# Kernel optimization log

Hardware: AMD Instinct MI355X
Metric: run time of the kernel (lower is better)

## Reference

```python
import jax, jax.numpy as jnp
import numpy as np

B, S, D = 4, 2048, 1024
E, K, H = 8, 2, 2048  # experts, top_k, swiglu hidden (ff_multiplier=2.0)
EPS = 1e-8
RMS_EPS = 1e-6
ROPE_BASE = 10000.0


def setup_inputs() -> dict:
    key = jax.random.key(0)
    ks = jax.random.split(key, 6)
    scale_in = 1.0 / np.sqrt(D)
    scale_h = 1.0 / np.sqrt(H)
    return {
        "x": jax.random.normal(ks[0], (B, S, D), jnp.float32),
        "norm_w": jnp.ones((D,), jnp.float32),
        "router_W": jax.random.normal(ks[1], (E, D), jnp.float32) * scale_in,  # nn.Linear weight [E,D]
        "w1": jax.random.normal(ks[2], (E, H, D), jnp.float32) * scale_in,  # gate proj per expert
        "w3": jax.random.normal(ks[3], (E, H, D), jnp.float32) * scale_in,  # up proj per expert
        "w2": jax.random.normal(ks[4], (E, D, H), jnp.float32) * scale_h,   # down proj per expert
    }


def _rmsnorm(x, w):
    var = jnp.mean(jnp.square(x), axis=-1, keepdims=True)
    return x * jax.lax.rsqrt(var + RMS_EPS) * w


def _rope(x):
    # half-split rotary embedding over full embed dim; x: [B,S,D]
    d2 = D // 2
    inv_freq = 1.0 / (ROPE_BASE ** (jnp.arange(0, d2, dtype=jnp.float32) / d2))
    ang = jnp.arange(S, dtype=jnp.float32)[:, None] * inv_freq[None, :]  # [S,D/2]
    cos, sin = jnp.cos(ang), jnp.sin(ang)
    x1, x2 = x[..., :d2], x[..., d2:]
    return jnp.concatenate([x1 * cos - x2 * sin, x1 * sin + x2 * cos], axis=-1)


def reference(x, norm_w, router_W, w1, w3, w2):
    hidden = _rope(_rmsnorm(x, norm_w))  # [B,S,D]
    logits = jnp.einsum("bsd,ed->bse", hidden, router_W)
    probs = jax.nn.softmax(logits, axis=-1)
    # sparse top-k renormalized gates
    top_v, top_i = jax.lax.top_k(probs, K)  # [B,S,K]
    sparse = jnp.sum(jax.nn.one_hot(top_i, E, dtype=probs.dtype) * top_v[..., None], axis=-2)  # [B,S,E]
    gates = sparse / jnp.clip(jnp.sum(sparse, axis=-1, keepdims=True), EPS)
    # dense all-expert SwiGLU
    g = jnp.einsum("bsd,ehd->bseh", hidden, w1)
    u = jnp.einsum("bsd,ehd->bseh", hidden, w3)
    act = jax.nn.silu(g) * u
    expert_out = jnp.einsum("bseh,edh->bsed", act, w2)  # [B,S,E,D]
    mixed = jnp.sum(gates[..., None] * expert_out, axis=-2)
    return mixed + x
```

## Files before the change

### kernel.cpp

```cpp
#include <hip/hip_runtime.h>

#define TOKENS 8192
#define Dm 1024
#define Hm 2048
#define Sm 2048
#define D2 512
#define SLOTS 16384
#define PADU 128
#define SLOTPAD (SLOTS + 8*PADU)
#define NWE 16777216

#define OF_TAB 0ull
#define OF_HID (OF_TAB + (size_t)Sm*D2*8)
#define OF_ACT (OF_HID + (size_t)TOKENS*Dm*2)
#define OF_W1B (OF_ACT + (size_t)SLOTPAD*Hm*2)
#define OF_W3B (OF_W1B + (size_t)NWE*2)
#define OF_W2B (OF_W3B + (size_t)NWE*2)
#define OF_T2I (OF_W2B + (size_t)NWE*2)
#define OF_T2G (OF_T2I + (size_t)TOKENS*2*4)
#define OF_T2S (OF_T2G + (size_t)TOKENS*2*4)
#define OF_ST  (OF_T2S + (size_t)TOKENS*2*4)
#define OF_SG  (OF_ST + (size_t)SLOTPAD*4)
#define OF_MT  (OF_SG + (size_t)SLOTPAD*4)
#define OF_SO  (OF_MT + 1024)

typedef __bf16 bf16x8 __attribute__((ext_vector_type(8)));
typedef short  s16x8  __attribute__((ext_vector_type(8)));
typedef float  f32x4  __attribute__((ext_vector_type(4)));

__device__ __forceinline__ unsigned short f2bf(float f) {
    union { float f; unsigned u; } v; v.f = f;
    unsigned r = v.u + 0x7fffu + ((v.u >> 16) & 1u);
    return (unsigned short)(r >> 16);
}

__device__ __forceinline__ float bf2f(unsigned short u) {
    union { unsigned u; float f; } v; v.u = ((unsigned)u) << 16;
    return v.f;
}

__device__ __forceinline__ f32x4 mfma16(s16x8 a, s16x8 b, f32x4 c) {
    return __builtin_amdgcn_mfma_f32_16x16x32_bf16(
        __builtin_bit_cast(bf16x8, a), __builtin_bit_cast(bf16x8, b), c, 0, 0, 0);
}

__device__ __forceinline__ void gld16(const void* g, void* l) {
    __builtin_amdgcn_global_load_lds(
        (const __attribute__((address_space(1))) void*)g,
        (__attribute__((address_space(3))) void*)l, 16, 0, 0);
}

__device__ __forceinline__ int xcd_swz(int bid, int nwg) {
    int cpx = nwg >> 3;
    return (bid & 7) * cpx + (bid >> 3);
}

__global__ void k_init(int* slot_token, int* meta) {
    int i = blockIdx.x * 256 + threadIdx.x;
    if (i < SLOTPAD) slot_token[i] = -1;
    if (i < 8) meta[i] = 0;
}

__global__ __launch_bounds__(256) void k_convert3(
    const float* __restrict__ w1, const float* __restrict__ w3,
    const float* __restrict__ w2, unsigned short* __restrict__ d1,
    unsigned short* __restrict__ d3, unsigned short* __restrict__ d2)
{
    size_t i = ((size_t)blockIdx.x * 256 + threadIdx.x) * 8;
    const float* s; unsigned short* d;
    if (i < (size_t)NWE)            { s = w1; d = d1; }
    else if (i < 2ull * NWE)        { s = w3; d = d3; i -= (size_t)NWE; }
    else                            { s = w2; d = d2; i -= 2ull * NWE; }
    float4 a = *(const float4*)(s + i);
    float4 b = *(const float4*)(s + i + 4);
    s16x8 v;
    v[0]=(short)f2bf(a.x); v[1]=(short)f2bf(a.y); v[2]=(short)f2bf(a.z); v[3]=(short)f2bf(a.w);
    v[4]=(short)f2bf(b.x); v[5]=(short)f2bf(b.y); v[6]=(short)f2bf(b.z); v[7]=(short)f2bf(b.w);
    *(s16x8*)(d + i) = v;
}

__global__ void k_table(float2* tab) {
    int i = blockIdx.x * 256 + threadIdx.x;
    int s = i >> 9, j = i & 511;
    float inv = expf(-(float)j * (9.210340371976184f / 512.0f));
    float ang = (float)s * inv;
    tab[i] = make_float2(cosf(ang), sinf(ang));
}

__global__ __launch_bounds__(256) void k_token(
    const float* __restrict__ x, const float* __restrict__ nw,
    const float* __restrict__ rW, const float2* __restrict__ tab,
    unsigned short* __restrict__ hid,
    int* __restrict__ t2i, float* __restrict__ t2g)
{
    int t = blockIdx.x;
    int tid = threadIdx.x;
    int lane = tid & 63, wid = tid >> 6;
    int s = t & (Sm - 1);
    const float* xr = x + (size_t)t * Dm;

    float v0 = xr[tid], v1 = xr[tid + 256], v2 = xr[tid + 512], v3 = xr[tid + 768];
    float ss = v0*v0 + v1*v1 + v2*v2 + v3*v3;
    #pragma unroll
    for (int o = 32; o; o >>= 1) ss += __shfl_down(ss, o);
    __shared__ float red[4];
    if (lane == 0) red[wid] = ss;
    __syncthreads();
    float tot = red[0] + red[1] + red[2] + red[3];
    float rms = rsqrtf(tot * (1.0f / Dm) + 1e-6f);

    float n0 = v0 * rms * nw[tid];
    float n1 = v1 * rms * nw[tid + 256];
    float n2 = v2 * rms * nw[tid + 512];
    float n3 = v3 * rms * nw[tid + 768];

    float2 c0 = tab[s * D2 + tid];
    float2 c1 = tab[s * D2 + tid + 256];
    float h0 = n0 * c0.x - n2 * c0.y;
    float h2 = n0 * c0.y + n2 * c0.x;
    float h1 = n1 * c1.x - n3 * c1.y;
    float h3 = n1 * c1.y + n3 * c1.x;

    size_t base = (size_t)t * Dm;
    hid[base + tid]       = f2bf(h0);
    hid[base + tid + 256] = f2bf(h1);
    hid[base + tid + 512] = f2bf(h2);
    hid[base + tid + 768] = f2bf(h3);

    float p[8];
    #pragma unroll
    for (int e = 0; e < 8; e++) {
        const float* r = rW + (size_t)e * Dm;
        p[e] = h0 * r[tid] + h1 * r[tid + 256] + h2 * r[tid + 512] + h3 * r[tid + 768];
    }
    #pragma unroll
    for (int e = 0; e < 8; e++)
        #pragma unroll
        for (int o = 32; o; o >>= 1) p[e] += __shfl_down(p[e], o);
    __shared__ float rl[4][8];
    if (lane == 0) {
        #pragma unroll
        for (int e = 0; e < 8; e++) rl[wid][e] = p[e];
    }
    __syncthreads();
    if (tid == 0) {
        float lg[8];
        #pragma unroll
        for (int e = 0; e < 8; e++) lg[e] = rl[0][e] + rl[1][e] + rl[2][e] + rl[3][e];
        float m = lg[0];
        #pragma unroll
        for (int e = 1; e < 8; e++) m = fmaxf(m, lg[e]);
        int i0 = 0; float b0 = lg[0];
        #pragma unroll
        for (int e = 1; e < 8; e++) if (lg[e] > b0) { b0 = lg[e]; i0 = e; }
        int i1 = -1; float b1 = -3.0e38f;
        #pragma unroll
        for (int e = 0; e < 8; e++) if (e != i0 && lg[e] > b1) { b1 = lg[e]; i1 = e; }
        float p0 = expf(b0 - m), p1 = expf(b1 - m);
        float inv = 1.0f / (p0 + p1);
        t2i[2 * t] = i0; t2i[2 * t + 1] = i1;
        t2g[2 * t] = p0 * inv; t2g[2 * t + 1] = p1 * inv;
    }
}

__global__ __launch_bounds__(256) void k_hist(const int* __restrict__ t2i,
                                              int* __restrict__ meta) {
    __shared__ int h[8];
    int tid = threadIdx.x;
    if (tid < 8) h[tid] = 0;
    __syncthreads();
    int base = blockIdx.x * 512 + tid * 2;
    atomicAdd(&h[t2i[base]], 1);
    atomicAdd(&h[t2i[base + 1]], 1);
    __syncthreads();
    if (tid < 8) atomicAdd(&meta[tid], h[tid]);
}

__global__ void k_offsets(int* meta) {
    if (threadIdx.x == 0 && blockIdx.x == 0) {
        int acc = 0;
        for (int e = 0; e < 8; e++) {
            meta[8 + e] = acc;
            acc += ((meta[e] + PADU - 1) / PADU) * PADU;
        }
        meta[16] = acc;
        for (int e = 0; e < 8; e++) meta[17 + e] = meta[8 + e];
    }
}

__global__ __launch_bounds__(256) void k_place(
    const int* __restrict__ t2i, const float* __restrict__ t2g,
    int* __restrict__ slot_token, float* __restrict__ slot_gate,
    int* __restrict__ t2s, int* __restrict__ meta)
{
    __shared__ int lcnt[8];
    __shared__ int lbase[8];
    int tid = threadIdx.x;
    if (tid < 8) lcnt[tid] = 0;
    __syncthreads();
    int t = blockIdx.x * 256 + tid;
    int e0 = t2i[2 * t], e1 = t2i[2 * t + 1];
    int r0 = atomicAdd(&lcnt[e0], 1);
    int r1 = atomicAdd(&lcnt[e1], 1);
    __syncthreads();
    if (tid < 8) lbase[tid] = atomicAdd(&meta[17 + tid], lcnt[tid]);
    __syncthreads();
    int p0 = lbase[e0] + r0, p1 = lbase[e1] + r1;
    slot_token[p0] = t; slot_gate[p0] = t2g[2 * t];     t2s[2 * t]     = p0;
    slot_token[p1] = t; slot_gate[p1] = t2g[2 * t + 1]; t2s[2 * t + 1] = p1;
}

__global__ __launch_bounds__(256) void k_gemm1(
    const unsigned short* __restrict__ hid,
    const unsigned short* __restrict__ w1b, const unsigned short* __restrict__ w3b,
    const int* __restrict__ slot_token, unsigned short* __restrict__ act,
    const int* __restrict__ meta)
{
    int nwg = gridDim.x * gridDim.y;
    int bid = blockIdx.y * gridDim.x + blockIdx.x;
    int wg  = xcd_swz(bid, nwg);
    int bx  = wg % gridDim.x, by = wg / gridDim.x;

    int row0 = by * 128;
    if (row0 >= meta[16]) return;
    int e = 0;
    #pragma unroll
    for (int q = 1; q < 8; q++) if (row0 >= meta[8 + q]) e = q;
    int h0 = bx * 64;

    __shared__ unsigned short As[2][128 * 64];
    __shared__ unsigned short Bs[2][128 * 64];

    int tid = threadIdx.x, lane = tid & 63, w = tid >> 6;
    int wm = w >> 1, wn = w & 1;
    int frow = lane & 15, q4 = lane >> 4;
    int rx = frow & 7;

    int r7 = (tid >> 3) & 7;
    int sslot = (tid & 7) ^ r7;

    const unsigned short* srcA[4];
    const unsigned short* srcB[4];
    #pragma unroll
    for (int i = 0; i < 4; i++) {
        int ra = i * 32 + (tid >> 3);
        int tok = slot_token[row0 + ra];     if (tok < 0) tok = 0;
        srcA[i] = hid + (size_t)tok * Dm + sslot * 8;
        int rb = i * 32 + (tid >> 3);
        if (rb < 64) srcB[i] = w1b + ((size_t)e * Hm + h0 + rb) * Dm + sslot * 8;
        else         srcB[i] = w3b + ((size_t)e * Hm + h0 + rb - 64) * Dm + sslot * 8;
    }

    f32x4 accG[4][2] = {};
    f32x4 accU[4][2] = {};

#define STAGE1(buf, k0) do {                                                  \
    unsigned short* la_ = &As[(buf)][tid * 8];                                \
    unsigned short* lb_ = &Bs[(buf)][tid * 8];                                \
    _Pragma("unroll")                                                         \
    for (int i_ = 0; i_ < 4; i_++) {                                          \
        gld16(srcA[i_] + (k0), la_ + i_ * 2048);                              \
        gld16(srcB[i_] + (k0), lb_ + i_ * 2048);                              \
    } } while (0)

#define COMP1(buf) do {                                                       \
    _Pragma("unroll")                                                         \
    for (int h_ = 0; h_ < 2; h_++) {                                          \
        int sp_ = ((h_ << 2) | q4) ^ rx;                                      \
        s16x8 am_[4], bg_[2], bu_[2];                                         \
        _Pragma("unroll")                                                     \
        for (int i_ = 0; i_ < 4; i_++)                                        \
            am_[i_] = *(const s16x8*)&As[(buf)][(wm * 64 + i_ * 16 + frow) * 64 + sp_ * 8]; \
        _Pragma("unroll")                                                     \
        for (int j_ = 0; j_ < 2; j_++) {                                      \
            bg_[j_] = *(const s16x8*)&Bs[(buf)][(wn * 32 + j_ * 16 + frow) * 64 + sp_ * 8]; \
            bu_[j_] = *(const s16x8*)&Bs[(buf)][(64 + wn * 32 + j_ * 16 + frow) * 64 + sp_ * 8]; \
        }                                                                     \
        _Pragma("unroll")                                                     \
        for (int i_ = 0; i_ < 4; i_++)                                        \
            _Pragma("unroll")                                                 \
            for (int j_ = 0; j_ < 2; j_++) {                                  \
                accG[i_][j_] = mfma16(am_[i_], bg_[j_], accG[i_][j_]);        \
                accU[i_][j_] = mfma16(am_[i_], bu_[j_], accU[i_][j_]);        \
            }                                                                 \
    } } while (0)

    STAGE1(0, 0);
    #pragma unroll 2
    for (int kt = 0; kt < 15; ++kt) {
        STAGE1((kt + 1) & 1, (kt + 1) * 64);
        asm volatile("s_waitcnt vmcnt(8)" ::: "memory");
        __builtin_amdgcn_s_barrier();
        __builtin_amdgcn_sched_barrier(0);
        COMP1(kt & 1);
        __builtin_amdgcn_sched_barrier(0);
        __builtin_amdgcn_s_barrier();
    }
    asm volatile("s_waitcnt vmcnt(0)" ::: "memory");
    __builtin_amdgcn_s_barrier();
    __builtin_amdgcn_sched_barrier(0);
    COMP1(1);

#undef STAGE1
#undef COMP1

    #pragma unroll
    for (int i = 0; i < 4; i++)
        #pragma unroll
        for (int j = 0; j < 2; j++)
            #pragma unroll
            for (int r = 0; r < 4; r++) {
                int sr = row0 + wm * 64 + i * 16 + q4 * 4 + r;
                int hc = h0 + wn * 32 + j * 16 + frow;
                float g = accG[i][j][r], u = accU[i][j][r];
                float a = g / (1.0f + expf(-g)) * u;
                act[(size_t)sr * Hm + hc] = f2bf(a);
            }
}

__global__ __launch_bounds__(256) void k_gemm2(
    const unsigned short* __restrict__ act, const unsigned short* __restrict__ w2b,
    const float* __restrict__ slot_gate,
    unsigned short* __restrict__ sout, const int* __restrict__ meta)
{
    int nwg = gridDim.x * gridDim.y;
    int bid = blockIdx.y * gridDim.x + blockIdx.x;
    int wg  = xcd_swz(bid, nwg);
    int bx  = wg % gridDim.x, by = wg / gridDim.x;

    int row0 = by * 128;
    if (row0 >= meta[16]) return;
    int e = 0;
    #pragma unroll
    for (int q = 1; q < 8; q++) if (row0 >= meta[8 + q]) e = q;
    int d0 = bx * 128;

    __shared__ unsigned short As[2][128 * 64];
    __shared__ unsigned short Bs[2][128 * 64];
    __shared__ float sgat[128];

    int tid = threadIdx.x, lane = tid & 63, w = tid >> 6;
    int wm = w >> 1, wn = w & 1;
    int frow = lane & 15, q4 = lane >> 4;
    int rx = frow & 7;

    if (tid < 128) sgat[tid] = slot_gate[row0 + tid];

    int r7 = (tid >> 3) & 7;
    int sslot = (tid & 7) ^ r7;

    const unsigned short* srcA[4];
    const unsigned short* srcB[4];
    #pragma unroll
    for (int i = 0; i < 4; i++) {
        int rr = i * 32 + (tid >> 3);
        srcA[i] = act + (size_t)(row0 + rr) * Hm + sslot * 8;
        srcB[i] = w2b + ((size_t)e * Dm + d0 + rr) * Hm + sslot * 8;
    }

    f32x4 acc[4][4] = {};

#define STAGE2(buf, k0) do {                                                  \
    unsigned short* la_ = &As[(buf)][tid * 8];                                \
    unsigned short* lb_ = &Bs[(buf)][tid * 8];                                \
    _Pragma("unroll")                                                         \
    for (int i_ = 0; i_ < 4; i_++) {                                          \
        gld16(srcA[i_] + (k0), la_ + i_ * 2048);                              \
        gld16(srcB[i_] + (k0), lb_ + i_ * 2048);                              \
    } } while (0)

#define COMP2(buf) do {                                                       \
    _Pragma("unroll")                                                         \
    for (int h_ = 0; h_ < 2; h_++) {                                          \
        int sp_ = ((h_ << 2) | q4) ^ rx;                                      \
        s16x8 am_[4], bn_[4];                                                 \
        _Pragma("unroll")                                                     \
        for (int i_ = 0; i_ < 4; i_++)                                        \
            am_[i_] = *(const s16x8*)&As[(buf)][(wm * 64 + i_ * 16 + frow) * 64 + sp_ * 8]; \
        _Pragma("unroll")                                                     \
        for (int j_ = 0; j_ < 4; j_++)                                        \
            bn_[j_] = *(const s16x8*)&Bs[(buf)][(wn * 64 + j_ * 16 + frow) * 64 + sp_ * 8]; \
        _Pragma("unroll")                                                     \
        for (int i_ = 0; i_ < 4; i_++)                                        \
            _Pragma("unroll")                                                 \
            for (int j_ = 0; j_ < 4; j_++)                                    \
                acc[i_][j_] = mfma16(am_[i_], bn_[j_], acc[i_][j_]);          \
    } } while (0)

    STAGE2(0, 0);
    #pragma unroll 2
    for (int kt = 0; kt < 31; ++kt) {
        STAGE2((kt + 1) & 1, (kt + 1) * 64);
        asm volatile("s_waitcnt vmcnt(8)" ::: "memory");
        __builtin_amdgcn_s_barrier();
        __builtin_amdgcn_sched_barrier(0);
        COMP2(kt & 1);
        __builtin_amdgcn_sched_barrier(0);
        __builtin_amdgcn_s_barrier();
    }
    asm volatile("s_waitcnt vmcnt(0)" ::: "memory");
    __builtin_amdgcn_s_barrier();
    __builtin_amdgcn_sched_barrier(0);
    COMP2(1);

#undef STAGE2
#undef COMP2

    #pragma unroll
    for (int i = 0; i < 4; i++) {
        #pragma unroll
        for (int r = 0; r < 4; r++) {
            int srl = wm * 64 + i * 16 + q4 * 4 + r;
            float gate = sgat[srl];
            size_t rb = (size_t)(row0 + srl) * Dm;
            #pragma unroll
            for (int j = 0; j < 4; j++) {
                int dc = d0 + wn * 64 + j * 16 + frow;
                sout[rb + dc] = f2bf(gate * acc[i][j][r]);
            }
        }
    }
}

__global__ __launch_bounds__(256) void k_final(
    const float* __restrict__ x, const unsigned short* __restrict__ sout,
    const int* __restrict__ t2s, float* __restrict__ out)
{
    int t = blockIdx.x;
    int tid = threadIdx.x;
    int s0 = t2s[2 * t], s1 = t2s[2 * t + 1];
    const float4*  xr = (const float4*)(x + (size_t)t * Dm);
    const ushort4* a  = (const ushort4*)(sout + (size_t)s0 * Dm);
    const ushort4* b  = (const ushort4*)(sout + (size_t)s1 * Dm);
    float4* o = (float4*)(out + (size_t)t * Dm);
    float4 xv = xr[tid];
    ushort4 av = a[tid], bv = b[tid];
    float4 r;
    r.x = xv.x + bf2f(av.x) + bf2f(bv.x);
    r.y = xv.y + bf2f(av.y) + bf2f(bv.y);
    r.z = xv.z + bf2f(av.z) + bf2f(bv.z);
    r.w = xv.w + bf2f(av.w) + bf2f(bv.w);
    o[tid] = r;
}

extern "C" void kernel_launch(void* const* d_in, const int* in_sizes, int n_in,
                              void* d_out, int out_size, void* d_ws, size_t ws_size,
                              hipStream_t stream) {
    const float* x  = (const float*)d_in[0];
    const float* nw = (const float*)d_in[1];
    const float* rW = (const float*)d_in[2];
    const float* w1 = (const float*)d_in[3];
    const float* w3 = (const float*)d_in[4];
    const float* w2 = (const float*)d_in[5];
    float* out = (float*)d_out;
    char* ws = (char*)d_ws;

    float2* tab = (float2*)(ws + OF_TAB);
    unsigned short* hid = (unsigned short*)(ws + OF_HID);
    unsigned short* act = (unsigned short*)(ws + OF_ACT);
    unsigned short* w1b = (unsigned short*)(ws + OF_W1B);
    unsigned short* w3b = (unsigned short*)(ws + OF_W3B);
    unsigned short* w2b = (unsigned short*)(ws + OF_W2B);
    int*   t2i  = (int*)(ws + OF_T2I);
    float* t2g  = (float*)(ws + OF_T2G);
    int*   t2s  = (int*)(ws + OF_T2S);
    int*   stok = (int*)(ws + OF_ST);
    float* sgat = (float*)(ws + OF_SG);
    int*   meta = (int*)(ws + OF_MT);
    unsigned short* sout = (unsigned short*)(ws + OF_SO);

    k_init<<<(SLOTPAD + 255) / 256, 256, 0, stream>>>(stok, meta);
    k_table<<<(Sm * D2) / 256, 256, 0, stream>>>(tab);
    k_convert3<<<3 * (NWE / (256 * 8)), 256, 0, stream>>>(w1, w3, w2, w1b, w3b, w2b);
    k_token<<<TOKENS, 256, 0, stream>>>(x, nw, rW, tab, hid, t2i, t2g);
    k_hist<<<32, 256, 0, stream>>>(t2i, meta);
    k_offsets<<<1, 64, 0, stream>>>(meta);
    k_place<<<TOKENS / 256, 256, 0, stream>>>(t2i, t2g, stok, sgat, t2s, meta);

    dim3 g1(Hm / 64, SLOTPAD / 128);
    k_gemm1<<<g1, 256, 0, stream>>>(hid, w1b, w3b, stok, act, meta);
    dim3 g2(Dm / 128, SLOTPAD / 128);
    k_gemm2<<<g2, 256, 0, stream>>>(act, w2b, sgat, sout, meta);
    k_final<<<TOKENS, 256, 0, stream>>>(x, sout, t2s, out);
}
```

Baseline: 385.7 us.

## Enlarge gemm1 tile to 256x128 with 8 waves and phased MFMA/load interleave

Grows the gate/up GEMM block tile from 128 rows x 64 hidden to 256 rows x 128 hidden using 512 threads (8 waves). Each wave now computes a 128x32 sub-tile, which raises data reuse per LDS byte. The K loop is split into four phases that interleave global-to-LDS prefetch with MFMA groups, bracketed by barriers and s_setprio. Expert padding grows to 256 rows to match the new row tile, which adds padded work per expert. LDS use doubles to 128KB, and register pressure rises from the larger accumulator set.

```diff
diff --git a/kernel.cpp b/kernel.cpp
--- a/kernel.cpp
+++ b/kernel.cpp
@@ -6,7 +6,7 @@
 #define Sm 2048
 #define D2 512
 #define SLOTS 16384
-#define PADU 128
+#define PADU 256
 #define SLOTPAD (SLOTS + 8*PADU)
 #define NWE 16777216
 
@@ -210,7 +210,7 @@
     slot_token[p1] = t; slot_gate[p1] = t2g[2 * t + 1]; t2s[2 * t + 1] = p1;
 }
 
-__global__ __launch_bounds__(256) void k_gemm1(
+__global__ __launch_bounds__(512) void k_gemm1(
     const unsigned short* __restrict__ hid,
     const unsigned short* __restrict__ w1b, const unsigned short* __restrict__ w3b,
     const int* __restrict__ slot_token, unsigned short* __restrict__ act,
@@ -221,98 +221,120 @@
     int wg  = xcd_swz(bid, nwg);
     int bx  = wg % gridDim.x, by = wg / gridDim.x;
 
-    int row0 = by * 128;
+    int row0 = by * 256;
     if (row0 >= meta[16]) return;
     int e = 0;
     #pragma unroll
     for (int q = 1; q < 8; q++) if (row0 >= meta[8 + q]) e = q;
-    int h0 = bx * 64;
-
-    __shared__ unsigned short As[2][128 * 64];
-    __shared__ unsigned short Bs[2][128 * 64];
+    int h0 = bx * 128;
+
+    __shared__ unsigned short As[2][256 * 64];
+    __shared__ unsigned short Bs[2][256 * 64];
 
     int tid = threadIdx.x, lane = tid & 63, w = tid >> 6;
-    int wm = w >> 1, wn = w & 1;
+    int wm = w >> 2, wn = w & 3;
+    int wrow = wm * 128, wcol = wn * 32;
     int frow = lane & 15, q4 = lane >> 4;
     int rx = frow & 7;
 
-    int r7 = (tid >> 3) & 7;
-    int sslot = (tid & 7) ^ r7;
+    int grow = tid >> 3;
+    int sslot = (tid & 7) ^ (grow & 7);
 
     const unsigned short* srcA[4];
     const unsigned short* srcB[4];
     #pragma unroll
-    for (int i = 0; i < 4; i++) {
-        int ra = i * 32 + (tid >> 3);
-        int tok = slot_token[row0 + ra];     if (tok < 0) tok = 0;
-        srcA[i] = hid + (size_t)tok * Dm + sslot * 8;
-        int rb = i * 32 + (tid >> 3);
-        if (rb < 64) srcB[i] = w1b + ((size_t)e * Hm + h0 + rb) * Dm + sslot * 8;
-        else         srcB[i] = w3b + ((size_t)e * Hm + h0 + rb - 64) * Dm + sslot * 8;
-    }
-
-    f32x4 accG[4][2] = {};
-    f32x4 accU[4][2] = {};
-
-#define STAGE1(buf, k0) do {                                                  \
-    unsigned short* la_ = &As[(buf)][tid * 8];                                \
-    unsigned short* lb_ = &Bs[(buf)][tid * 8];                                \
-    _Pragma("unroll")                                                         \
-    for (int i_ = 0; i_ < 4; i_++) {                                          \
-        gld16(srcA[i_] + (k0), la_ + i_ * 2048);                              \
-        gld16(srcB[i_] + (k0), lb_ + i_ * 2048);                              \
+    for (int g = 0; g < 4; g++) {
+        int ra = g * 64 + grow;
+        int tok = slot_token[row0 + ra];  if (tok < 0) tok = 0;
+        srcA[g] = hid + (size_t)tok * Dm + sslot * 8;
+        int rb = g * 64 + grow;
+        srcB[g] = (rb < 128 ? w1b + ((size_t)e * Hm + h0 + rb) * Dm
+                            : w3b + ((size_t)e * Hm + h0 + rb - 128) * Dm) + sslot * 8;
+    }
+
+    s16x8 a8[4][2], bG[2][2], bU[2][2];
+    f32x4 accG[8][2] = {};
+    f32x4 accU[8][2] = {};
+
+#define SA(nb, g) gld16(srcA[g] + koff, (unsigned short*)&As[(nb)][(g) * 4096 + tid * 8])
+#define SB(nb, g) gld16(srcB[g] + koff, (unsigned short*)&Bs[(nb)][(g) * 4096 + tid * 8])
+
+#define RD_A(buf, half) do {                                                  \
+    _Pragma("unroll") for (int i_ = 0; i_ < 4; i_++)                          \
+    _Pragma("unroll") for (int kh_ = 0; kh_ < 2; kh_++) {                     \
+        int sp_ = ((kh_ << 2) | q4) ^ rx;                                     \
+        a8[i_][kh_] = *(const s16x8*)&As[(buf)][(wrow + (half) * 64 + i_ * 16 + frow) * 64 + sp_ * 8]; \
     } } while (0)
 
-#define COMP1(buf) do {                                                       \
-    _Pragma("unroll")                                                         \
-    for (int h_ = 0; h_ < 2; h_++) {                                          \
-        int sp_ = ((h_ << 2) | q4) ^ rx;                                      \
-        s16x8 am_[4], bg_[2], bu_[2];                                         \
-        _Pragma("unroll")                                                     \
-        for (int i_ = 0; i_ < 4; i_++)                                        \
-            am_[i_] = *(const s16x8*)&As[(buf)][(wm * 64 + i_ * 16 + frow) * 64 + sp_ * 8]; \
-        _Pragma("unroll")                                                     \
-        for (int j_ = 0; j_ < 2; j_++) {                                      \
-            bg_[j_] = *(const s16x8*)&Bs[(buf)][(wn * 32 + j_ * 16 + frow) * 64 + sp_ * 8]; \
-            bu_[j_] = *(const s16x8*)&Bs[(buf)][(64 + wn * 32 + j_ * 16 + frow) * 64 + sp_ * 8]; \
-        }                                                                     \
-        _Pragma("unroll")                                                     \
-        for (int i_ = 0; i_ < 4; i_++)                                        \
-            _Pragma("unroll")                                                 \
-            for (int j_ = 0; j_ < 2; j_++) {                                  \
-                accG[i_][j_] = mfma16(am_[i_], bg_[j_], accG[i_][j_]);        \
-                accU[i_][j_] = mfma16(am_[i_], bu_[j_], accU[i_][j_]);        \
-            }                                                                 \
+#define RD_B(buf, arr, base) do {                                             \
+    _Pragma("unroll") for (int j_ = 0; j_ < 2; j_++)                          \
+    _Pragma("unroll") for (int kh_ = 0; kh_ < 2; kh_++) {                     \
+        int sp_ = ((kh_ << 2) | q4) ^ rx;                                     \
+        arr[j_][kh_] = *(const s16x8*)&Bs[(buf)][((base) + wcol + j_ * 16 + frow) * 64 + sp_ * 8]; \
     } } while (0)
 
-    STAGE1(0, 0);
-    #pragma unroll 2
-    for (int kt = 0; kt < 15; ++kt) {
-        STAGE1((kt + 1) & 1, (kt + 1) * 64);
-        asm volatile("s_waitcnt vmcnt(8)" ::: "memory");
+#define MFMA_Q(accX, bX, half) do {                                           \
+    _Pragma("unroll") for (int i_ = 0; i_ < 4; i_++)                          \
+    _Pragma("unroll") for (int j_ = 0; j_ < 2; j_++)                          \
+    _Pragma("unroll") for (int kh_ = 0; kh_ < 2; kh_++)                       \
+        accX[(half) * 4 + i_][j_] = mfma16(a8[i_][kh_], bX[j_][kh_], accX[(half) * 4 + i_][j_]); \
+    } while (0)
+
+#define PH_PRE  do { __builtin_amdgcn_s_barrier();                            \
+    asm volatile("s_waitcnt lgkmcnt(0)" ::: "memory");                        \
+    __builtin_amdgcn_sched_barrier(0);                                        \
+    __builtin_amdgcn_s_setprio(1); } while (0)
+#define PH_POST do { __builtin_amdgcn_s_setprio(0);                           \
+    __builtin_amdgcn_s_barrier(); } while (0)
+
+    {
+        int koff = 0;
+        #pragma unroll
+        for (int g = 0; g < 4; g++) SA(0, g);
+        #pragma unroll
+        for (int g = 0; g < 4; g++) SB(0, g);
+        asm volatile("s_waitcnt vmcnt(0)" ::: "memory");
+        __builtin_amdgcn_s_barrier();
+    }
+
+    for (int kt = 0; kt < 16; ++kt) {
+        int buf = kt & 1, nbuf = buf ^ 1;
+        int koff = (kt + 1) * 64;
+        bool st = kt < 15;
+        RD_A(buf, 0); RD_B(buf, bG, 0);
+        if (st) { SA(nbuf, 0); SA(nbuf, 1); SA(nbuf, 2); }
+        PH_PRE; MFMA_Q(accG, bG, 0); PH_POST;
+        RD_B(buf, bU, 128);
+        if (st) { SA(nbuf, 3); SB(nbuf, 0); SB(nbuf, 1); }
+        PH_PRE; MFMA_Q(accU, bU, 0); PH_POST;
+        RD_A(buf, 1);
+        if (st) { SB(nbuf, 2); SB(nbuf, 3); }
+        PH_PRE; MFMA_Q(accG, bG, 1); PH_POST;
+        __builtin_amdgcn_s_setprio(1);
+        MFMA_Q(accU, bU, 1);
+        __builtin_amdgcn_s_setprio(0);
+        asm volatile("s_waitcnt vmcnt(0)" ::: "memory");
         __builtin_amdgcn_s_barrier();
         __builtin_amdgcn_sched_barrier(0);
-        COMP1(kt & 1);
-        __builtin_amdgcn_sched_barrier(0);
-        __builtin_amdgcn_s_barrier();
-    }
-    asm volatile("s_waitcnt vmcnt(0)" ::: "memory");
-    __builtin_amdgcn_s_barrier();
-    __builtin_amdgcn_sched_barrier(0);
-    COMP1(1);
-
-#undef STAGE1
-#undef COMP1
-
-    #pragma unroll
-    for (int i = 0; i < 4; i++)
+    }
+
+#undef SA
+#undef SB
+#undef RD_A
+#undef RD_B
+#undef MFMA_Q
+#undef PH_PRE
+#undef PH_POST
+
+    #pragma unroll
+    for (int m = 0; m < 8; m++)
         #pragma unroll
         for (int j = 0; j < 2; j++)
             #pragma unroll
             for (int r = 0; r < 4; r++) {
-                int sr = row0 + wm * 64 + i * 16 + q4 * 4 + r;
-                int hc = h0 + wn * 32 + j * 16 + frow;
-                float g = accG[i][j][r], u = accU[i][j][r];
+                int sr = row0 + wrow + m * 16 + q4 * 4 + r;
+                int hc = h0 + wcol + j * 16 + frow;
+                float g = accG[m][j][r], u = accU[m][j][r];
                 float a = g / (1.0f + expf(-g)) * u;
                 act[(size_t)sr * Hm + hc] = f2bf(a);
             }
@@ -477,8 +499,8 @@
     k_offsets<<<1, 64, 0, stream>>>(meta);
     k_place<<<TOKENS / 256, 256, 0, stream>>>(t2i, t2g, stok, sgat, t2s, meta);
 
-    dim3 g1(Hm / 64, SLOTPAD / 128);
-    k_gemm1<<<g1, 256, 0, stream>>>(hid, w1b, w3b, stok, act, meta);
+    dim3 g1(Hm / 128, SLOTPAD / 256);
+    k_gemm1<<<g1, 512, 0, stream>>>(hid, w1b, w3b, stok, act, meta);
     dim3 g2(Dm / 128, SLOTPAD / 128);
     k_gemm2<<<g2, 256, 0, stream>>>(act, w2b, sgat, sout, meta);
     k_final<<<TOKENS, 256, 0, stream>>>(x, sout, t2s, out);
```

Result: no change. 383.0 us (-0.7%).

## Fuse prep kernels into one launch, inline RoPE trig, halve gemm1 K-tile

Applied to the files above, without the earlier changes.

Merges the init, weight-conversion and token (RMSNorm+RoPE+router) kernels into a single launch dispatched by block index. The RoPE cos/sin table is now computed inline per token instead of by a separate table kernel. gemm1's K tile is halved from 64 to 32, which halves LDS use and lets the launch bounds request 4 blocks per CU for higher occupancy, at the cost of twice as many loop iterations and barriers. Recomputing the trig per token adds transcendental work in exchange for skipping the table writes and reads.

```diff
diff --git a/kernel.cpp b/kernel.cpp
--- a/kernel.cpp
+++ b/kernel.cpp
@@ -24,6 +24,10 @@
 #define OF_MT  (OF_SG + (size_t)SLOTPAD*4)
 #define OF_SO  (OF_MT + 1024)
 
+#define PREP_TOKEN 8192
+#define PREP_CONV  (PREP_TOKEN + 3 * (NWE / (256 * 8)))
+#define PREP_INIT  (PREP_CONV + (SLOTPAD + 255) / 256)
+
 typedef __bf16 bf16x8 __attribute__((ext_vector_type(8)));
 typedef short  s16x8  __attribute__((ext_vector_type(8)));
 typedef float  f32x4  __attribute__((ext_vector_type(4)));
@@ -55,46 +59,44 @@
     return (bid & 7) * cpx + (bid >> 3);
 }
 
-__global__ void k_init(int* slot_token, int* meta) {
-    int i = blockIdx.x * 256 + threadIdx.x;
-    if (i < SLOTPAD) slot_token[i] = -1;
-    if (i < 8) meta[i] = 0;
-}
-
-__global__ __launch_bounds__(256) void k_convert3(
+__global__ __launch_bounds__(256) void k_prep(
+    const float* __restrict__ x, const float* __restrict__ nw,
+    const float* __restrict__ rW,
     const float* __restrict__ w1, const float* __restrict__ w3,
-    const float* __restrict__ w2, unsigned short* __restrict__ d1,
-    unsigned short* __restrict__ d3, unsigned short* __restrict__ d2)
+    const float* __restrict__ w2,
+    unsigned short* __restrict__ hid, int* __restrict__ t2i,
+    float* __restrict__ t2g,
+    unsigned short* __restrict__ d1, unsigned short* __restrict__ d3,
+    unsigned short* __restrict__ d2,
+    int* __restrict__ slot_token, int* __restrict__ meta)
 {
-    size_t i = ((size_t)blockIdx.x * 256 + threadIdx.x) * 8;
-    const float* s; unsigned short* d;
-    if (i < (size_t)NWE)            { s = w1; d = d1; }
-    else if (i < 2ull * NWE)        { s = w3; d = d3; i -= (size_t)NWE; }
-    else                            { s = w2; d = d2; i -= 2ull * NWE; }
-    float4 a = *(const float4*)(s + i);
-    float4 b = *(const float4*)(s + i + 4);
-    s16x8 v;
-    v[0]=(short)f2bf(a.x); v[1]=(short)f2bf(a.y); v[2]=(short)f2bf(a.z); v[3]=(short)f2bf(a.w);
-    v[4]=(short)f2bf(b.x); v[5]=(short)f2bf(b.y); v[6]=(short)f2bf(b.z); v[7]=(short)f2bf(b.w);
-    *(s16x8*)(d + i) = v;
-}
-
-__global__ void k_table(float2* tab) {
-    int i = blockIdx.x * 256 + threadIdx.x;
-    int s = i >> 9, j = i & 511;
-    float inv = expf(-(float)j * (9.210340371976184f / 512.0f));
-    float ang = (float)s * inv;
-    tab[i] = make_float2(cosf(ang), sinf(ang));
-}
-
-__global__ __launch_bounds__(256) void k_token(
-    const float* __restrict__ x, const float* __restrict__ nw,
-    const float* __restrict__ rW, const float2* __restrict__ tab,
-    unsigned short* __restrict__ hid,
-    int* __restrict__ t2i, float* __restrict__ t2g)
-{
-    int t = blockIdx.x;
+    __shared__ float red[4];
+    __shared__ float rl[4][8];
+    int bid = blockIdx.x;
     int tid = threadIdx.x;
+
+    if (bid >= PREP_CONV) {
+        int i = (bid - PREP_CONV) * 256 + tid;
+        if (i < SLOTPAD) slot_token[i] = -1;
+        if (i < 8) meta[i] = 0;
+        return;
+    }
+    if (bid >= PREP_TOKEN) {
+        size_t i = ((size_t)(bid - PREP_TOKEN) * 256 + tid) * 8;
+        const float* s; unsigned short* d;
+        if (i < (size_t)NWE)            { s = w1; d = d1; }
+        else if (i < 2ull * NWE)        { s = w3; d = d3; i -= (size_t)NWE; }
+        else                            { s = w2; d = d2; i -= 2ull * NWE; }
+        float4 a = *(const float4*)(s + i);
+        float4 b = *(const float4*)(s + i + 4);
+        s16x8 v;
+        v[0]=(short)f2bf(a.x); v[1]=(short)f2bf(a.y); v[2]=(short)f2bf(a.z); v[3]=(short)f2bf(a.w);
+        v[4]=(short)f2bf(b.x); v[5]=(short)f2bf(b.y); v[6]=(short)f2bf(b.z); v[7]=(short)f2bf(b.w);
+        *(s16x8*)(d + i) = v;
+        return;
+    }
+
+    int t = bid;
     int lane = tid & 63, wid = tid >> 6;
     int s = t & (Sm - 1);
     const float* xr = x + (size_t)t * Dm;
@@ -103,7 +105,6 @@
     float ss = v0*v0 + v1*v1 + v2*v2 + v3*v3;
     #pragma unroll
     for (int o = 32; o; o >>= 1) ss += __shfl_down(ss, o);
-    __shared__ float red[4];
     if (lane == 0) red[wid] = ss;
     __syncthreads();
     float tot = red[0] + red[1] + red[2] + red[3];
@@ -114,12 +115,15 @@
     float n2 = v2 * rms * nw[tid + 512];
     float n3 = v3 * rms * nw[tid + 768];
 
-    float2 c0 = tab[s * D2 + tid];
-    float2 c1 = tab[s * D2 + tid + 256];
-    float h0 = n0 * c0.x - n2 * c0.y;
-    float h2 = n0 * c0.y + n2 * c0.x;
-    float h1 = n1 * c1.x - n3 * c1.y;
-    float h3 = n1 * c1.y + n3 * c1.x;
+    const float kk = -0.017988946039016842f;
+    float a0 = (float)s * expf((float)tid * kk);
+    float a1 = (float)s * expf((float)(tid + 256) * kk);
+    float c0x = cosf(a0), c0y = sinf(a0);
+    float c1x = cosf(a1), c1y = sinf(a1);
+    float h0 = n0 * c0x - n2 * c0y;
+    float h2 = n0 * c0y + n2 * c0x;
+    float h1 = n1 * c1x - n3 * c1y;
+    float h3 = n1 * c1y + n3 * c1x;
 
     size_t base = (size_t)t * Dm;
     hid[base + tid]       = f2bf(h0);
@@ -137,7 +141,6 @@
     for (int e = 0; e < 8; e++)
         #pragma unroll
         for (int o = 32; o; o >>= 1) p[e] += __shfl_down(p[e], o);
-    __shared__ float rl[4][8];
     if (lane == 0) {
         #pragma unroll
         for (int e = 0; e < 8; e++) rl[wid][e] = p[e];
@@ -210,7 +213,7 @@
     slot_token[p1] = t; slot_gate[p1] = t2g[2 * t + 1]; t2s[2 * t + 1] = p1;
 }
 
-__global__ __launch_bounds__(256) void k_gemm1(
+__global__ __launch_bounds__(256, 4) void k_gemm1(
     const unsigned short* __restrict__ hid,
     const unsigned short* __restrict__ w1b, const unsigned short* __restrict__ w3b,
     const int* __restrict__ slot_token, unsigned short* __restrict__ act,
@@ -228,81 +231,74 @@
     for (int q = 1; q < 8; q++) if (row0 >= meta[8 + q]) e = q;
     int h0 = bx * 64;
 
-    __shared__ unsigned short As[2][128 * 64];
-    __shared__ unsigned short Bs[2][128 * 64];
+    __shared__ unsigned short As[2][128 * 32];
+    __shared__ unsigned short Bs[2][128 * 32];
 
     int tid = threadIdx.x, lane = tid & 63, w = tid >> 6;
     int wm = w >> 1, wn = w & 1;
     int frow = lane & 15, q4 = lane >> 4;
-    int rx = frow & 7;
-
-    int r7 = (tid >> 3) & 7;
-    int sslot = (tid & 7) ^ r7;
-
-    const unsigned short* srcA[4];
-    const unsigned short* srcB[4];
-    #pragma unroll
-    for (int i = 0; i < 4; i++) {
-        int ra = i * 32 + (tid >> 3);
-        int tok = slot_token[row0 + ra];     if (tok < 0) tok = 0;
-        srcA[i] = hid + (size_t)tok * Dm + sslot * 8;
-        int rb = i * 32 + (tid >> 3);
-        if (rb < 64) srcB[i] = w1b + ((size_t)e * Hm + h0 + rb) * Dm + sslot * 8;
-        else         srcB[i] = w3b + ((size_t)e * Hm + h0 + rb - 64) * Dm + sslot * 8;
-    }
+    int rx = frow & 3;
+
+    int srow = tid >> 2;
+    int sslot = (tid & 3) ^ (srow & 3);
+
+    const unsigned short* srcA[2];
+    #pragma unroll
+    for (int g = 0; g < 2; g++) {
+        int tok = slot_token[row0 + g * 64 + srow];  if (tok < 0) tok = 0;
+        srcA[g] = hid + (size_t)tok * Dm + sslot * 8;
+    }
+    const unsigned short* srcB0 = w1b + ((size_t)e * Hm + h0 + srow) * Dm + sslot * 8;
+    const unsigned short* srcB1 = w3b + ((size_t)e * Hm + h0 + srow) * Dm + sslot * 8;
 
     f32x4 accG[4][2] = {};
     f32x4 accU[4][2] = {};
 
-#define STAGE1(buf, k0) do {                                                  \
-    unsigned short* la_ = &As[(buf)][tid * 8];                                \
-    unsigned short* lb_ = &Bs[(buf)][tid * 8];                                \
+#define ST1(nb, k0) do {                                                      \
+    gld16(srcA[0] + (k0), (unsigned short*)&As[(nb)][tid * 8]);               \
+    gld16(srcA[1] + (k0), (unsigned short*)&As[(nb)][2048 + tid * 8]);        \
+    gld16(srcB0   + (k0), (unsigned short*)&Bs[(nb)][tid * 8]);               \
+    gld16(srcB1   + (k0), (unsigned short*)&Bs[(nb)][2048 + tid * 8]);        \
+    } while (0)
+
+#define CP1(buf) do {                                                         \
+    int sp_ = q4 ^ rx;                                                        \
+    s16x8 am_[4], bg_[2], bu_[2];                                             \
     _Pragma("unroll")                                                         \
-    for (int i_ = 0; i_ < 4; i_++) {                                          \
-        gld16(srcA[i_] + (k0), la_ + i_ * 2048);                              \
-        gld16(srcB[i_] + (k0), lb_ + i_ * 2048);                              \
-    } } while (0)
-
-#define COMP1(buf) do {                                                       \
+    for (int i_ = 0; i_ < 4; i_++)                                            \
+        am_[i_] = *(const s16x8*)&As[(buf)][(wm * 64 + i_ * 16 + frow) * 32 + sp_ * 8]; \
     _Pragma("unroll")                                                         \
-    for (int h_ = 0; h_ < 2; h_++) {                                          \
-        int sp_ = ((h_ << 2) | q4) ^ rx;                                      \
-        s16x8 am_[4], bg_[2], bu_[2];                                         \
-        _Pragma("unroll")                                                     \
-        for (int i_ = 0; i_ < 4; i_++)                                        \
-            am_[i_] = *(const s16x8*)&As[(buf)][(wm * 64 + i_ * 16 + frow) * 64 + sp_ * 8]; \
+    for (int j_ = 0; j_ < 2; j_++) {                                          \
+        bg_[j_] = *(const s16x8*)&Bs[(buf)][(wn * 32 + j_ * 16 + frow) * 32 + sp_ * 8]; \
+        bu_[j_] = *(const s16x8*)&Bs[(buf)][(64 + wn * 32 + j_ * 16 + frow) * 32 + sp_ * 8]; \
+    }                                                                         \
+    _Pragma("unroll")                                                         \
+    for (int i_ = 0; i_ < 4; i_++)                                            \
         _Pragma("unroll")                                                     \
         for (int j_ = 0; j_ < 2; j_++) {                                      \
-            bg_[j_] = *(const s16x8*)&Bs[(buf)][(wn * 32 + j_ * 16 + frow) * 64 + sp_ * 8]; \
-            bu_[j_] = *(const s16x8*)&Bs[(buf)][(64 + wn * 32 + j_ * 16 + frow) * 64 + sp_ * 8]; \
+            accG[i_][j_] = mfma16(am_[i_], bg_[j_], accG[i_][j_]);            \
+            accU[i_][j_] = mfma16(am_[i_], bu_[j_], accU[i_][j_]);            \
         }                                                                     \
-        _Pragma("unroll")                                                     \
-        for (int i_ = 0; i_ < 4; i_++)                                        \
-            _Pragma("unroll")                                                 \
-            for (int j_ = 0; j_ < 2; j_++) {                                  \
-                accG[i_][j_] = mfma16(am_[i_], bg_[j_], accG[i_][j_]);        \
-                accU[i_][j_] = mfma16(am_[i_], bu_[j_], accU[i_][j_]);        \
-            }                                                                 \
-    } } while (0)
-
-    STAGE1(0, 0);
+    } while (0)
+
+    ST1(0, 0);
     #pragma unroll 2
-    for (int kt = 0; kt < 15; ++kt) {
-        STAGE1((kt + 1) & 1, (kt + 1) * 64);
-        asm volatile("s_waitcnt vmcnt(8)" ::: "memory");
+    for (int kt = 0; kt < 31; ++kt) {
+        ST1((kt + 1) & 1, (kt + 1) * 32);
+        asm volatile("s_waitcnt vmcnt(4)" ::: "memory");
         __builtin_amdgcn_s_barrier();
         __builtin_amdgcn_sched_barrier(0);
-        COMP1(kt & 1);
+        CP1(kt & 1);
         __builtin_amdgcn_sched_barrier(0);
         __builtin_amdgcn_s_barrier();
     }
     asm volatile("s_waitcnt vmcnt(0)" ::: "memory");
     __builtin_amdgcn_s_barrier();
     __builtin_amdgcn_sched_barrier(0);
-    COMP1(1);
-
-#undef STAGE1
-#undef COMP1
+    CP1(1);
+
+#undef ST1
+#undef CP1
 
     #pragma unroll
     for (int i = 0; i < 4; i++)
@@ -455,7 +451,6 @@
     float* out = (float*)d_out;
     char* ws = (char*)d_ws;
 
-    float2* tab = (float2*)(ws + OF_TAB);
     unsigned short* hid = (unsigned short*)(ws + OF_HID);
     unsigned short* act = (unsigned short*)(ws + OF_ACT);
     unsigned short* w1b = (unsigned short*)(ws + OF_W1B);
@@ -469,10 +464,9 @@
     int*   meta = (int*)(ws + OF_MT);
     unsigned short* sout = (unsigned short*)(ws + OF_SO);
 
-    k_init<<<(SLOTPAD + 255) / 256, 256, 0, stream>>>(stok, meta);
-    k_table<<<(Sm * D2) / 256, 256, 0, stream>>>(tab);
-    k_convert3<<<3 * (NWE / (256 * 8)), 256, 0, stream>>>(w1, w3, w2, w1b, w3b, w2b);
-    k_token<<<TOKENS, 256, 0, stream>>>(x, nw, rW, tab, hid, t2i, t2g);
+    k_prep<<<PREP_INIT, 256, 0, stream>>>(x, nw, rW, w1, w3, w2,
+                                          hid, t2i, t2g, w1b, w3b, w2b,
+                                          stok, meta);
     k_hist<<<32, 256, 0, stream>>>(t2i, meta);
     k_offsets<<<1, 64, 0, stream>>>(meta);
     k_place<<<TOKENS / 256, 256, 0, stream>>>(t2i, t2g, stok, sgat, t2s, meta);
```

After: 366.7 us. -4.9%, faster.
